# Kernel tuning notes

Hardware: AMD Instinct MI355X
Metric: run time of the kernel (lower is better)

The kernel has to match this reference:

```python
import jax, jax.numpy as jnp
import numpy as np

WS = 8          # window size
NH = 8          # num heads
EPS = 1e-5      # LayerNorm eps (torch default)


def setup_inputs() -> dict:
    key = jax.random.key(0)
    ks = jax.random.split(key, 7)
    B, C, H, W = 16, 256, 128, 128
    x = jax.random.normal(ks[0], (B, C, H, W), dtype=jnp.float32)
    ln_gamma = jnp.ones((C,), dtype=jnp.float32)
    ln_beta = jnp.zeros((C,), dtype=jnp.float32)
    s = 1.0 / np.sqrt(C)
    w_in = jax.random.uniform(ks[1], (3 * C, C), jnp.float32, -s, s)
    b_in = jnp.zeros((3 * C,), dtype=jnp.float32)
    w_out = jax.random.uniform(ks[2], (C, C), jnp.float32, -s, s)
    b_out = jnp.zeros((C,), dtype=jnp.float32)
    return {"x": x, "ln_gamma": ln_gamma, "ln_beta": ln_beta,
            "w_in": w_in, "b_in": b_in, "w_out": w_out, "b_out": b_out}


def _layernorm(x, gamma, beta):
    mu = jnp.mean(x, axis=-1, keepdims=True)
    var = jnp.mean(jnp.square(x - mu), axis=-1, keepdims=True)
    return (x - mu) * jax.lax.rsqrt(var + EPS) * gamma + beta


def reference(x, ln_gamma, ln_beta, w_in, b_in, w_out, b_out):
    B, C, H, W = x.shape
    dh = C // NH
    N = WS * WS
    # (B,C,H,W) -> (B,H,W,C) -> windows (B*nW, N, C)
    xh = jnp.transpose(x, (0, 2, 3, 1))
    win = xh.reshape(B, H // WS, WS, W // WS, WS, C)
    win = jnp.transpose(win, (0, 1, 3, 2, 4, 5)).reshape(-1, N, C)
    # single LayerNorm (the torch code computes the same LN three times)
    xn = _layernorm(win, ln_gamma, ln_beta)
    # fused QKV projection
    qkv = xn @ w_in.T + b_in                      # (Bn, N, 3C)
    q, k, v = jnp.split(qkv, 3, axis=-1)
    def heads(t):
        return jnp.transpose(t.reshape(-1, N, NH, dh), (0, 2, 1, 3))  # (Bn,h,N,dh)
    q, k, v = heads(q), heads(k), heads(v)
    scores = jnp.einsum('bhnd,bhmd->bhnm', q, k) / jnp.sqrt(jnp.float32(dh))
    attn = jax.nn.softmax(scores, axis=-1)
    out = jnp.einsum('bhnm,bhmd->bhnd', attn, v)  # (Bn,h,N,dh)
    out = jnp.transpose(out, (0, 2, 1, 3)).reshape(-1, N, C)
    out = out @ w_out.T + b_out
    # window reverse -> (B,H,W,C) -> (B,C,H,W)
    out = out.reshape(B, H // WS, W // WS, WS, WS, C)
    out = jnp.transpose(out, (0, 1, 3, 2, 4, 5)).reshape(B, H, W, C)
    return jnp.transpose(out, (0, 3, 1, 2))
```

## Files before the change

### kernel.cpp

```cpp
#include <hip/hip_runtime.h>


typedef _Float16 half8  __attribute__((ext_vector_type(8)));
typedef _Float16 half2v __attribute__((ext_vector_type(2)));
typedef float    f32x4  __attribute__((ext_vector_type(4)));

#define XN_STR 264
#define XN_SZ  (64 * XN_STR)
#define S_STR  72
#define S_SZ   (64 * S_STR)
#define SM_TOT (XN_SZ + 4 * S_SZ)

__device__ __forceinline__ int xn_idx(int row, int c) {
    return row * XN_STR + (((c >> 3) ^ (row >> 3)) << 3) + (c & 7);
}
__device__ __forceinline__ int p_idx(int q, int k) {
    return q * 64 + (((k >> 3) ^ (q & 7)) << 3) + (k & 7);
}

__global__ void __launch_bounds__(256)
prep_weights_f16(const float* __restrict__ w_in, const float* __restrict__ w_out,
                 _Float16* __restrict__ wh) {
    int i = blockIdx.x * 256 + threadIdx.x;
    if (i < 196608)      wh[i] = (_Float16)w_in[i];
    else if (i < 262144) wh[i] = (_Float16)w_out[i - 196608];
}

__global__ void __launch_bounds__(256, 2)
win_attn_fused(const float* __restrict__ x, const float* __restrict__ gamma,
               const float* __restrict__ beta, const float* __restrict__ b_in,
               const float* __restrict__ b_out,
               const _Float16* __restrict__ w_in_h,
               const _Float16* __restrict__ w_out_h,
               float* __restrict__ out)
{
    __shared__ __align__(16) _Float16 sm[SM_TOT];
    __shared__ float s_gb[512];

    const int tid  = threadIdx.x;
    const int bidr = blockIdx.x;
    const int wid  = (bidr & 7) * 512 + (bidr >> 3);
    const int b    = wid >> 8;
    const int whi  = (wid >> 4) & 15;
    const int wwi  = wid & 15;
    const int h0 = whi * 8, w0 = wwi * 8;

    s_gb[tid]       = gamma[tid];
    s_gb[256 + tid] = beta[tid];

    const int wv   = tid >> 6;
    const int lane = tid & 63;
    const int quad = lane >> 4;
    const int l16  = lane & 15;

    {
        const int th = lane & 7;
        const int qq = (lane >> 3) & 1;
        const int cg = wv * 4 + (lane >> 4);
        const int t0 = th * 8 + qq * 4;
        const float* xb = x + (((size_t)b * 256) * 128 + h0) * 128 + w0;
#pragma unroll
        for (int it = 0; it < 16; ++it) {
            int c = it * 16 + cg;
            float4 v = *(const float4*)(xb + ((size_t)c * 128 + th) * 128 + qq * 4);
            int base = t0 * XN_STR + (((c >> 3) ^ th) << 3) + (c & 7);
            sm[base]              = (_Float16)v.x;
            sm[base + XN_STR]     = (_Float16)v.y;
            sm[base + 2 * XN_STR] = (_Float16)v.z;
            sm[base + 3 * XN_STR] = (_Float16)v.w;
        }
    }
    __syncthreads();

    {
        const int tok = tid >> 2, cq = tid & 3;
        float sum = 0.f, ss = 0.f;
        half8 hv[8];
#pragma unroll
        for (int k2 = 0; k2 < 8; ++k2) {
            hv[k2] = *(const half8*)&sm[xn_idx(tok, cq * 64 + k2 * 8)];
#pragma unroll
            for (int j = 0; j < 8; ++j) { float f = (float)hv[k2][j]; sum += f; ss += f * f; }
        }
        sum += __shfl_xor(sum, 1); ss += __shfl_xor(ss, 1);
        sum += __shfl_xor(sum, 2); ss += __shfl_xor(ss, 2);
        float mu   = sum * (1.f / 256.f);
        float var  = ss * (1.f / 256.f) - mu * mu;
        float rstd = rsqrtf(var + 1e-5f);
#pragma unroll
        for (int k2 = 0; k2 < 8; ++k2) {
            int c0 = cq * 64 + k2 * 8;
            float4 g0 = *(const float4*)&s_gb[c0];
            float4 g1 = *(const float4*)&s_gb[c0 + 4];
            float4 e0 = *(const float4*)&s_gb[256 + c0];
            float4 e1 = *(const float4*)&s_gb[256 + c0 + 4];
            float gg[8] = {g0.x, g0.y, g0.z, g0.w, g1.x, g1.y, g1.z, g1.w};
            float bb[8] = {e0.x, e0.y, e0.z, e0.w, e1.x, e1.y, e1.z, e1.w};
            half8 o;
#pragma unroll
            for (int j = 0; j < 8; ++j)
                o[j] = (_Float16)(((float)hv[k2][j] - mu) * rstd * gg[j] + bb[j]);
            *(half8*)&sm[xn_idx(tok, c0)] = o;
        }
    }
    __syncthreads();

    const f32x4 zero4 = {0.f, 0.f, 0.f, 0.f};
    _Float16* Swv = &sm[XN_SZ + wv * S_SZ];

    auto qkv_pass = [&](const int p, f32x4 (&acc)[4][4]) {
#pragma unroll
        for (int mt = 0; mt < 4; ++mt)
#pragma unroll
            for (int nt = 0; nt < 4; ++nt) acc[mt][nt] = zero4;
        const _Float16* wb = w_in_h + (size_t)(p * 256 + wv * 64) * 256 + quad * 8;
#pragma unroll
        for (int kb = 0; kb < 256; kb += 32) {
            half8 af[4], bf[4];
#pragma unroll
            for (int mt = 0; mt < 4; ++mt)
                af[mt] = *(const half8*)&sm[xn_idx(mt * 16 + l16, kb + quad * 8)];
#pragma unroll
            for (int nt = 0; nt < 4; ++nt)
                bf[nt] = *(const half8*)(wb + (size_t)(nt * 16 + l16) * 256 + kb);
#pragma unroll
            for (int mt = 0; mt < 4; ++mt)
#pragma unroll
                for (int nt = 0; nt < 4; ++nt)
                    acc[mt][nt] = __builtin_amdgcn_mfma_f32_16x16x32_f16(af[mt], bf[nt], acc[mt][nt], 0, 0, 0);
        }
#pragma unroll
        for (int nt = 0; nt < 4; ++nt) {
            float bi = b_in[p * 256 + wv * 64 + nt * 16 + l16];
#pragma unroll
            for (int mt = 0; mt < 4; ++mt) {
                acc[mt][nt][0] += bi; acc[mt][nt][1] += bi;
                acc[mt][nt][2] += bi; acc[mt][nt][3] += bi;
            }
        }
    };

    half8 qfrag[2][4], kfrag[2][4];

    {
        f32x4 acc[4][4];
        qkv_pass(0, acc);
#pragma unroll
        for (int mt = 0; mt < 4; ++mt)
#pragma unroll
            for (int nt = 0; nt < 4; ++nt)
#pragma unroll
                for (int r = 0; r < 4; ++r)
                    Swv[(mt * 16 + quad * 4 + r) * S_STR + nt * 16 + l16] = (_Float16)acc[mt][nt][r];
        asm volatile("s_waitcnt lgkmcnt(0)" ::: "memory");
        __builtin_amdgcn_sched_barrier(0);
#pragma unroll
        for (int hh = 0; hh < 2; ++hh)
#pragma unroll
            for (int nt = 0; nt < 4; ++nt)
                qfrag[hh][nt] = *(const half8*)&Swv[(nt * 16 + l16) * S_STR + hh * 32 + quad * 8];
    }
    asm volatile("s_waitcnt lgkmcnt(0)" ::: "memory");
    __builtin_amdgcn_sched_barrier(0);

    {
        f32x4 acc[4][4];
        qkv_pass(1, acc);
#pragma unroll
        for (int mt = 0; mt < 4; ++mt)
#pragma unroll
            for (int nt = 0; nt < 4; ++nt)
#pragma unroll
                for (int r = 0; r < 4; ++r)
                    Swv[(mt * 16 + quad * 4 + r) * S_STR + nt * 16 + l16] = (_Float16)acc[mt][nt][r];
        asm volatile("s_waitcnt lgkmcnt(0)" ::: "memory");
        __builtin_amdgcn_sched_barrier(0);
#pragma unroll
        for (int hh = 0; hh < 2; ++hh)
#pragma unroll
            for (int nt = 0; nt < 4; ++nt)
                kfrag[hh][nt] = *(const half8*)&Swv[(nt * 16 + l16) * S_STR + hh * 32 + quad * 8];
    }
    asm volatile("s_waitcnt lgkmcnt(0)" ::: "memory");
    __builtin_amdgcn_sched_barrier(0);

    {
        f32x4 acc[4][4];
        qkv_pass(2, acc);
#pragma unroll
        for (int mt = 0; mt < 4; ++mt)
#pragma unroll
            for (int nt = 0; nt < 4; ++nt)
#pragma unroll
                for (int rp = 0; rp < 2; ++rp) {
                    half2v pk = { (_Float16)acc[mt][nt][2 * rp], (_Float16)acc[mt][nt][2 * rp + 1] };
                    *(half2v*)&Swv[(nt * 16 + l16) * S_STR + mt * 16 + quad * 4 + 2 * rp] = pk;
                }
    }
    __syncthreads();

    f32x4 oacc[2][2][4];
    float rs[2][4];
    _Float16* Pw = &sm[wv * 4096];

#pragma unroll
    for (int hh = 0; hh < 2; ++hh) {
        f32x4 s[4][4];
#pragma unroll
        for (int mt = 0; mt < 4; ++mt)
#pragma unroll
            for (int nt = 0; nt < 4; ++nt)
                s[mt][nt] = __builtin_amdgcn_mfma_f32_16x16x32_f16(kfrag[hh][mt], qfrag[hh][nt], zero4, 0, 0, 0);

        const float SC = 0.17677669529663687f * 1.4426950408889634f;
#pragma unroll
        for (int nt = 0; nt < 4; ++nt) {
            float m = -3.0e38f;
#pragma unroll
            for (int mt = 0; mt < 4; ++mt)
#pragma unroll
                for (int r = 0; r < 4; ++r) m = fmaxf(m, s[mt][nt][r]);
            m = fmaxf(m, __shfl_xor(m, 16));
            m = fmaxf(m, __shfl_xor(m, 32));
            float sum = 0.f;
#pragma unroll
            for (int mt = 0; mt < 4; ++mt)
#pragma unroll
                for (int r = 0; r < 4; ++r) {
                    float e = exp2f((s[mt][nt][r] - m) * SC);
                    s[mt][nt][r] = e; sum += e;
                }
            sum += __shfl_xor(sum, 16);
            sum += __shfl_xor(sum, 32);
            rs[hh][nt] = 1.f / sum;
        }

#pragma unroll
        for (int nt = 0; nt < 4; ++nt) {
            int q = nt * 16 + l16;
#pragma unroll
            for (int mt = 0; mt < 4; ++mt) {
                int k0 = mt * 16 + quad * 4;
                int a0 = p_idx(q, k0);
                half2v lo = { (_Float16)s[mt][nt][0], (_Float16)s[mt][nt][1] };
                half2v hi = { (_Float16)s[mt][nt][2], (_Float16)s[mt][nt][3] };
                *(half2v*)&Pw[a0]     = lo;
                *(half2v*)&Pw[a0 + 2] = hi;
            }
        }
        asm volatile("s_waitcnt lgkmcnt(0)" ::: "memory");
        __builtin_amdgcn_sched_barrier(0);

#pragma unroll
        for (int mtv = 0; mtv < 2; ++mtv)
#pragma unroll
            for (int nt = 0; nt < 4; ++nt) oacc[hh][mtv][nt] = zero4;
#pragma unroll
        for (int kb = 0; kb < 2; ++kb) {
            half8 av[2], bp[4];
#pragma unroll
            for (int mtv = 0; mtv < 2; ++mtv)
                av[mtv] = *(const half8*)&Swv[(hh * 32 + mtv * 16 + l16) * S_STR + kb * 32 + quad * 8];
#pragma unroll
            for (int nt = 0; nt < 4; ++nt)
                bp[nt] = *(const half8*)&Pw[p_idx(nt * 16 + l16, kb * 32 + quad * 8)];
#pragma unroll
            for (int mtv = 0; mtv < 2; ++mtv)
#pragma unroll
                for (int nt = 0; nt < 4; ++nt)
                    oacc[hh][mtv][nt] = __builtin_amdgcn_mfma_f32_16x16x32_f16(av[mtv], bp[nt], oacc[hh][mtv][nt], 0, 0, 0);
        }
    }
    __syncthreads();

#pragma unroll
    for (int hh = 0; hh < 2; ++hh)
#pragma unroll
        for (int mtv = 0; mtv < 2; ++mtv)
#pragma unroll
            for (int nt = 0; nt < 4; ++nt) {
                int tok = nt * 16 + l16;
                int c0  = (2 * wv + hh) * 32 + mtv * 16 + quad * 4;
                float sc = rs[hh][nt];
                int a0 = xn_idx(tok, c0);
                half2v lo = { (_Float16)(oacc[hh][mtv][nt][0] * sc), (_Float16)(oacc[hh][mtv][nt][1] * sc) };
                half2v hi = { (_Float16)(oacc[hh][mtv][nt][2] * sc), (_Float16)(oacc[hh][mtv][nt][3] * sc) };
                *(half2v*)&sm[a0]     = lo;
                *(half2v*)&sm[a0 + 2] = hi;
            }
    __syncthreads();

    f32x4 pacc[4][4];
#pragma unroll
    for (int mt = 0; mt < 4; ++mt)
#pragma unroll
        for (int nt = 0; nt < 4; ++nt) pacc[mt][nt] = zero4;
    const _Float16* wor = w_out_h + (size_t)(64 * wv + l16) * 256 + quad * 8;
#pragma unroll
    for (int kb = 0; kb < 256; kb += 32) {
        half8 aw[4], bo[4];
#pragma unroll
        for (int mt = 0; mt < 4; ++mt) aw[mt] = *(const half8*)(wor + mt * 16 * 256 + kb);
#pragma unroll
        for (int nt = 0; nt < 4; ++nt)
            bo[nt] = *(const half8*)&sm[xn_idx(nt * 16 + l16, kb + quad * 8)];
#pragma unroll
        for (int mt = 0; mt < 4; ++mt)
#pragma unroll
            for (int nt = 0; nt < 4; ++nt)
                pacc[mt][nt] = __builtin_amdgcn_mfma_f32_16x16x32_f16(aw[mt], bo[nt], pacc[mt][nt], 0, 0, 0);
    }

    float* ob = out + (((size_t)b * 256) * 128 + h0) * 128 + w0;
#pragma unroll
    for (int mt = 0; mt < 4; ++mt) {
#pragma unroll
        for (int r = 0; r < 4; ++r) {
            int c = 64 * wv + mt * 16 + quad * 4 + r;
            float bi = b_out[c];
#pragma unroll
            for (int nt = 0; nt < 4; ++nt) {
                int tok = nt * 16 + l16;
                ob[((size_t)c * 128 + (tok >> 3)) * 128 + (tok & 7)] = pacc[mt][nt][r] + bi;
            }
        }
    }
}

extern "C" void kernel_launch(void* const* d_in, const int* in_sizes, int n_in,
                              void* d_out, int out_size, void* d_ws, size_t ws_size,
                              hipStream_t stream) {
    const float* x        = (const float*)d_in[0];
    const float* ln_gamma = (const float*)d_in[1];
    const float* ln_beta  = (const float*)d_in[2];
    const float* w_in     = (const float*)d_in[3];
    const float* b_in     = (const float*)d_in[4];
    const float* w_out    = (const float*)d_in[5];
    const float* b_out    = (const float*)d_in[6];
    float* y = (float*)d_out;

    _Float16* w_in_h  = (_Float16*)d_ws;
    _Float16* w_out_h = w_in_h + 196608;

    prep_weights_f16<<<1024, 256, 0, stream>>>(w_in, w_out, w_in_h);
    win_attn_fused<<<4096, 256, 0, stream>>>(x, ln_gamma, ln_beta, b_in, b_out,
                                             w_in_h, w_out_h, y);
}
```

Before: 694.5 us.

## Replace LDS staging of Q/K/V/P with register ds_bpermute fragment shuffles

Q, K, V and softmax probabilities are rearranged into MFMA operand layouts through cross-lane ds_bpermute shuffles in registers, so the per-wave LDS scratch buffers and their write/read round-trips go away. This shrinks shared memory to the single normalized-activation tile, which lets launch bounds target three blocks per CU instead of two. Softmax normalization now happens before the PV product and attention is processed per head to keep fewer live accumulators. The cost is many extra bpermute instructions and higher register pressure, which could cause spills under the tighter occupancy bound.

```diff
diff --git a/kernel.cpp b/kernel.cpp
--- a/kernel.cpp
+++ b/kernel.cpp
@@ -7,15 +7,25 @@
 
 #define XN_STR 264
 #define XN_SZ  (64 * XN_STR)
-#define S_STR  72
-#define S_SZ   (64 * S_STR)
-#define SM_TOT (XN_SZ + 4 * S_SZ)
 
 __device__ __forceinline__ int xn_idx(int row, int c) {
     return row * XN_STR + (((c >> 3) ^ (row >> 3)) << 3) + (c & 7);
 }
-__device__ __forceinline__ int p_idx(int q, int k) {
-    return q * 64 + (((k >> 3) ^ (q & 7)) << 3) + (k & 7);
+
+__device__ __forceinline__ int pk2(float a, float b) {
+    half2v h = { (_Float16)a, (_Float16)b };
+    return __builtin_bit_cast(int, h);
+}
+
+__device__ __forceinline__ int qsel(bool hi, int idx, int lo_r, int hi_r) {
+    int a = __builtin_amdgcn_ds_bpermute(idx, lo_r);
+    int b = __builtin_amdgcn_ds_bpermute(idx, hi_r);
+    return hi ? b : a;
+}
+
+__device__ __forceinline__ half8 frag4(int w0, int w1, int w2, int w3) {
+    int4 t = { w0, w1, w2, w3 };
+    return __builtin_bit_cast(half8, t);
 }
 
 __global__ void __launch_bounds__(256)
@@ -26,7 +36,7 @@
     else if (i < 262144) wh[i] = (_Float16)w_out[i - 196608];
 }
 
-__global__ void __launch_bounds__(256, 2)
+__global__ void __launch_bounds__(256, 3)
 win_attn_fused(const float* __restrict__ x, const float* __restrict__ gamma,
                const float* __restrict__ beta, const float* __restrict__ b_in,
                const float* __restrict__ b_out,
@@ -34,7 +44,7 @@
                const _Float16* __restrict__ w_out_h,
                float* __restrict__ out)
 {
-    __shared__ __align__(16) _Float16 sm[SM_TOT];
+    __shared__ __align__(16) _Float16 sm[XN_SZ];
     __shared__ float s_gb[512];
 
     const int tid  = threadIdx.x;
@@ -56,18 +66,19 @@
     {
         const int th = lane & 7;
         const int qq = (lane >> 3) & 1;
-        const int cg = wv * 4 + (lane >> 4);
-        const int t0 = th * 8 + qq * 4;
+        const int cp = lane >> 4;
+        const int rowb = th * 8 + qq * 4;
         const float* xb = x + (((size_t)b * 256) * 128 + h0) * 128 + w0;
 #pragma unroll
-        for (int it = 0; it < 16; ++it) {
-            int c = it * 16 + cg;
-            float4 v = *(const float4*)(xb + ((size_t)c * 128 + th) * 128 + qq * 4);
-            int base = t0 * XN_STR + (((c >> 3) ^ th) << 3) + (c & 7);
-            sm[base]              = (_Float16)v.x;
-            sm[base + XN_STR]     = (_Float16)v.y;
-            sm[base + 2 * XN_STR] = (_Float16)v.z;
-            sm[base + 3 * XN_STR] = (_Float16)v.w;
+        for (int it = 0; it < 8; ++it) {
+            int c0 = it * 32 + wv * 8 + cp * 2;
+            float4 v0 = *(const float4*)(xb + ((size_t)c0 * 128 + th) * 128 + qq * 4);
+            float4 v1 = *(const float4*)(xb + ((size_t)(c0 + 1) * 128 + th) * 128 + qq * 4);
+            int base = rowb * XN_STR + (((c0 >> 3) ^ th) << 3) + (c0 & 7);
+            *(half2v*)&sm[base]              = half2v{ (_Float16)v0.x, (_Float16)v1.x };
+            *(half2v*)&sm[base + XN_STR]     = half2v{ (_Float16)v0.y, (_Float16)v1.y };
+            *(half2v*)&sm[base + 2 * XN_STR] = half2v{ (_Float16)v0.z, (_Float16)v1.z };
+            *(half2v*)&sm[base + 3 * XN_STR] = half2v{ (_Float16)v0.w, (_Float16)v1.w };
         }
     }
     __syncthreads();
@@ -90,204 +101,203 @@
 #pragma unroll
         for (int k2 = 0; k2 < 8; ++k2) {
             int c0 = cq * 64 + k2 * 8;
-            float4 g0 = *(const float4*)&s_gb[c0];
-            float4 g1 = *(const float4*)&s_gb[c0 + 4];
-            float4 e0 = *(const float4*)&s_gb[256 + c0];
-            float4 e1 = *(const float4*)&s_gb[256 + c0 + 4];
-            float gg[8] = {g0.x, g0.y, g0.z, g0.w, g1.x, g1.y, g1.z, g1.w};
-            float bb[8] = {e0.x, e0.y, e0.z, e0.w, e1.x, e1.y, e1.z, e1.w};
             half8 o;
 #pragma unroll
             for (int j = 0; j < 8; ++j)
-                o[j] = (_Float16)(((float)hv[k2][j] - mu) * rstd * gg[j] + bb[j]);
+                o[j] = (_Float16)(((float)hv[k2][j] - mu) * rstd * s_gb[c0 + j] + s_gb[256 + c0 + j]);
             *(half8*)&sm[xn_idx(tok, c0)] = o;
         }
     }
     __syncthreads();
 
     const f32x4 zero4 = {0.f, 0.f, 0.f, 0.f};
-    _Float16* Swv = &sm[XN_SZ + wv * S_SZ];
-
-    auto qkv_pass = [&](const int p, f32x4 (&acc)[4][4]) {
+    const int idxA = ((lane & 16) << 3) | ((lane & 15) << 2);
+    const int idxB = idxA + 64;
+    const bool hi2 = (lane & 32) != 0;
+
+    auto gemm_pass = [&](const int p, const bool xn_as_A, f32x4 (&acc)[4][4]) {
+#pragma unroll
+        for (int i = 0; i < 4; ++i)
+#pragma unroll
+            for (int j = 0; j < 4; ++j) acc[i][j] = zero4;
+        const _Float16* wb = w_in_h + ((size_t)(p * 256 + wv * 64 + l16)) * 256 + quad * 8;
+#pragma unroll
+        for (int kb = 0; kb < 8; ++kb) {
+            half8 wf[4], bx[4];
+#pragma unroll
+            for (int i = 0; i < 4; ++i)
+                wf[i] = *(const half8*)(wb + (size_t)i * 16 * 256 + kb * 32);
+#pragma unroll
+            for (int j = 0; j < 4; ++j)
+                bx[j] = *(const half8*)&sm[xn_idx(j * 16 + l16, kb * 32 + quad * 8)];
+            if (xn_as_A) {
+#pragma unroll
+                for (int i = 0; i < 4; ++i)
+#pragma unroll
+                    for (int j = 0; j < 4; ++j)
+                        acc[i][j] = __builtin_amdgcn_mfma_f32_16x16x32_f16(bx[i], wf[j], acc[i][j], 0, 0, 0);
+            } else {
+#pragma unroll
+                for (int i = 0; i < 4; ++i)
+#pragma unroll
+                    for (int j = 0; j < 4; ++j)
+                        acc[i][j] = __builtin_amdgcn_mfma_f32_16x16x32_f16(wf[i], bx[j], acc[i][j], 0, 0, 0);
+            }
+        }
+    };
+
+    half8 qfrag[2][4], kfrag[2][4], vfrag[2][2][2];
+
+    {
+        f32x4 acc[4][4];
+        gemm_pass(0, false, acc);
+#pragma unroll
+        for (int mt = 0; mt < 4; ++mt) {
+            f32x4 bq = *(const f32x4*)&b_in[0 * 256 + wv * 64 + mt * 16 + quad * 4];
+#pragma unroll
+            for (int nt = 0; nt < 4; ++nt) acc[mt][nt] += bq;
+        }
+        int pkq[4][4][2];
 #pragma unroll
         for (int mt = 0; mt < 4; ++mt)
 #pragma unroll
-            for (int nt = 0; nt < 4; ++nt) acc[mt][nt] = zero4;
-        const _Float16* wb = w_in_h + (size_t)(p * 256 + wv * 64) * 256 + quad * 8;
-#pragma unroll
-        for (int kb = 0; kb < 256; kb += 32) {
-            half8 af[4], bf[4];
+            for (int nt = 0; nt < 4; ++nt) {
+                pkq[mt][nt][0] = pk2(acc[mt][nt][0], acc[mt][nt][1]);
+                pkq[mt][nt][1] = pk2(acc[mt][nt][2], acc[mt][nt][3]);
+            }
+#pragma unroll
+        for (int hh = 0; hh < 2; ++hh)
+#pragma unroll
+            for (int nt = 0; nt < 4; ++nt)
+                qfrag[hh][nt] = frag4(
+                    qsel(hi2, idxA, pkq[2*hh][nt][0], pkq[2*hh+1][nt][0]),
+                    qsel(hi2, idxA, pkq[2*hh][nt][1], pkq[2*hh+1][nt][1]),
+                    qsel(hi2, idxB, pkq[2*hh][nt][0], pkq[2*hh+1][nt][0]),
+                    qsel(hi2, idxB, pkq[2*hh][nt][1], pkq[2*hh+1][nt][1]));
+    }
+
+    {
+        f32x4 acc[4][4];
+        gemm_pass(1, false, acc);
+#pragma unroll
+        for (int mt = 0; mt < 4; ++mt) {
+            f32x4 bk = *(const f32x4*)&b_in[1 * 256 + wv * 64 + mt * 16 + quad * 4];
+#pragma unroll
+            for (int nt = 0; nt < 4; ++nt) acc[mt][nt] += bk;
+        }
+        int pkk[4][4][2];
+#pragma unroll
+        for (int mt = 0; mt < 4; ++mt)
+#pragma unroll
+            for (int nt = 0; nt < 4; ++nt) {
+                pkk[mt][nt][0] = pk2(acc[mt][nt][0], acc[mt][nt][1]);
+                pkk[mt][nt][1] = pk2(acc[mt][nt][2], acc[mt][nt][3]);
+            }
+#pragma unroll
+        for (int hh = 0; hh < 2; ++hh)
+#pragma unroll
+            for (int nt = 0; nt < 4; ++nt)
+                kfrag[hh][nt] = frag4(
+                    qsel(hi2, idxA, pkk[2*hh][nt][0], pkk[2*hh+1][nt][0]),
+                    qsel(hi2, idxA, pkk[2*hh][nt][1], pkk[2*hh+1][nt][1]),
+                    qsel(hi2, idxB, pkk[2*hh][nt][0], pkk[2*hh+1][nt][0]),
+                    qsel(hi2, idxB, pkk[2*hh][nt][1], pkk[2*hh+1][nt][1]));
+    }
+
+    {
+        f32x4 acc[4][4];
+        gemm_pass(2, true, acc);
+#pragma unroll
+        for (int nt = 0; nt < 4; ++nt) {
+            float bv = b_in[2 * 256 + wv * 64 + nt * 16 + l16];
+            f32x4 bvv = { bv, bv, bv, bv };
+#pragma unroll
+            for (int mt = 0; mt < 4; ++mt) acc[mt][nt] += bvv;
+        }
+        int pkv[4][4][2];
+#pragma unroll
+        for (int mt = 0; mt < 4; ++mt)
+#pragma unroll
+            for (int nt = 0; nt < 4; ++nt) {
+                pkv[mt][nt][0] = pk2(acc[mt][nt][0], acc[mt][nt][1]);
+                pkv[mt][nt][1] = pk2(acc[mt][nt][2], acc[mt][nt][3]);
+            }
+        __syncthreads();
+#pragma unroll
+        for (int hh = 0; hh < 2; ++hh)
+#pragma unroll
+            for (int mtv = 0; mtv < 2; ++mtv)
+#pragma unroll
+                for (int kb = 0; kb < 2; ++kb)
+                    vfrag[hh][mtv][kb] = frag4(
+                        qsel(hi2, idxA, pkv[2*kb][2*hh+mtv][0], pkv[2*kb+1][2*hh+mtv][0]),
+                        qsel(hi2, idxA, pkv[2*kb][2*hh+mtv][1], pkv[2*kb+1][2*hh+mtv][1]),
+                        qsel(hi2, idxB, pkv[2*kb][2*hh+mtv][0], pkv[2*kb+1][2*hh+mtv][0]),
+                        qsel(hi2, idxB, pkv[2*kb][2*hh+mtv][1], pkv[2*kb+1][2*hh+mtv][1]));
+    }
+
+    const float SC = 0.17677669529663687f * 1.4426950408889634f;
+#pragma unroll
+    for (int hh = 0; hh < 2; ++hh) {
+        f32x4 oacc[2][4];
+#pragma unroll
+        for (int mtv = 0; mtv < 2; ++mtv)
+#pragma unroll
+            for (int nt = 0; nt < 4; ++nt) oacc[mtv][nt] = zero4;
+
+#pragma unroll
+        for (int nt = 0; nt < 4; ++nt) {
+            f32x4 s4[4];
 #pragma unroll
             for (int mt = 0; mt < 4; ++mt)
-                af[mt] = *(const half8*)&sm[xn_idx(mt * 16 + l16, kb + quad * 8)];
-#pragma unroll
-            for (int nt = 0; nt < 4; ++nt)
-                bf[nt] = *(const half8*)(wb + (size_t)(nt * 16 + l16) * 256 + kb);
+                s4[mt] = __builtin_amdgcn_mfma_f32_16x16x32_f16(kfrag[hh][mt], qfrag[hh][nt], zero4, 0, 0, 0);
+            float mx = -3.0e38f;
 #pragma unroll
             for (int mt = 0; mt < 4; ++mt)
 #pragma unroll
-                for (int nt = 0; nt < 4; ++nt)
-                    acc[mt][nt] = __builtin_amdgcn_mfma_f32_16x16x32_f16(af[mt], bf[nt], acc[mt][nt], 0, 0, 0);
-        }
-#pragma unroll
-        for (int nt = 0; nt < 4; ++nt) {
-            float bi = b_in[p * 256 + wv * 64 + nt * 16 + l16];
-#pragma unroll
-            for (int mt = 0; mt < 4; ++mt) {
-                acc[mt][nt][0] += bi; acc[mt][nt][1] += bi;
-                acc[mt][nt][2] += bi; acc[mt][nt][3] += bi;
-            }
-        }
-    };
-
-    half8 qfrag[2][4], kfrag[2][4];
-
-    {
-        f32x4 acc[4][4];
-        qkv_pass(0, acc);
-#pragma unroll
-        for (int mt = 0; mt < 4; ++mt)
-#pragma unroll
-            for (int nt = 0; nt < 4; ++nt)
-#pragma unroll
-                for (int r = 0; r < 4; ++r)
-                    Swv[(mt * 16 + quad * 4 + r) * S_STR + nt * 16 + l16] = (_Float16)acc[mt][nt][r];
-        asm volatile("s_waitcnt lgkmcnt(0)" ::: "memory");
-        __builtin_amdgcn_sched_barrier(0);
-#pragma unroll
-        for (int hh = 0; hh < 2; ++hh)
-#pragma unroll
-            for (int nt = 0; nt < 4; ++nt)
-                qfrag[hh][nt] = *(const half8*)&Swv[(nt * 16 + l16) * S_STR + hh * 32 + quad * 8];
-    }
-    asm volatile("s_waitcnt lgkmcnt(0)" ::: "memory");
-    __builtin_amdgcn_sched_barrier(0);
-
-    {
-        f32x4 acc[4][4];
-        qkv_pass(1, acc);
-#pragma unroll
-        for (int mt = 0; mt < 4; ++mt)
-#pragma unroll
-            for (int nt = 0; nt < 4; ++nt)
-#pragma unroll
-                for (int r = 0; r < 4; ++r)
-                    Swv[(mt * 16 + quad * 4 + r) * S_STR + nt * 16 + l16] = (_Float16)acc[mt][nt][r];
-        asm volatile("s_waitcnt lgkmcnt(0)" ::: "memory");
-        __builtin_amdgcn_sched_barrier(0);
-#pragma unroll
-        for (int hh = 0; hh < 2; ++hh)
-#pragma unroll
-            for (int nt = 0; nt < 4; ++nt)
-                kfrag[hh][nt] = *(const half8*)&Swv[(nt * 16 + l16) * S_STR + hh * 32 + quad * 8];
-    }
-    asm volatile("s_waitcnt lgkmcnt(0)" ::: "memory");
-    __builtin_amdgcn_sched_barrier(0);
-
-    {
-        f32x4 acc[4][4];
-        qkv_pass(2, acc);
-#pragma unroll
-        for (int mt = 0; mt < 4; ++mt)
-#pragma unroll
-            for (int nt = 0; nt < 4; ++nt)
-#pragma unroll
-                for (int rp = 0; rp < 2; ++rp) {
-                    half2v pk = { (_Float16)acc[mt][nt][2 * rp], (_Float16)acc[mt][nt][2 * rp + 1] };
-                    *(half2v*)&Swv[(nt * 16 + l16) * S_STR + mt * 16 + quad * 4 + 2 * rp] = pk;
-                }
-    }
-    __syncthreads();
-
-    f32x4 oacc[2][2][4];
-    float rs[2][4];
-    _Float16* Pw = &sm[wv * 4096];
-
-#pragma unroll
-    for (int hh = 0; hh < 2; ++hh) {
-        f32x4 s[4][4];
-#pragma unroll
-        for (int mt = 0; mt < 4; ++mt)
-#pragma unroll
-            for (int nt = 0; nt < 4; ++nt)
-                s[mt][nt] = __builtin_amdgcn_mfma_f32_16x16x32_f16(kfrag[hh][mt], qfrag[hh][nt], zero4, 0, 0, 0);
-
-        const float SC = 0.17677669529663687f * 1.4426950408889634f;
-#pragma unroll
-        for (int nt = 0; nt < 4; ++nt) {
-            float m = -3.0e38f;
+                for (int r = 0; r < 4; ++r) mx = fmaxf(mx, s4[mt][r]);
+            mx = fmaxf(mx, __shfl_xor(mx, 16));
+            mx = fmaxf(mx, __shfl_xor(mx, 32));
+            float sum = 0.f;
 #pragma unroll
             for (int mt = 0; mt < 4; ++mt)
 #pragma unroll
-                for (int r = 0; r < 4; ++r) m = fmaxf(m, s[mt][nt][r]);
-            m = fmaxf(m, __shfl_xor(m, 16));
-            m = fmaxf(m, __shfl_xor(m, 32));
-            float sum = 0.f;
-#pragma unroll
-            for (int mt = 0; mt < 4; ++mt)
-#pragma unroll
                 for (int r = 0; r < 4; ++r) {
-                    float e = exp2f((s[mt][nt][r] - m) * SC);
-                    s[mt][nt][r] = e; sum += e;
+                    float e = exp2f((s4[mt][r] - mx) * SC);
+                    s4[mt][r] = e; sum += e;
                 }
             sum += __shfl_xor(sum, 16);
             sum += __shfl_xor(sum, 32);
-            rs[hh][nt] = 1.f / sum;
-        }
-
-#pragma unroll
-        for (int nt = 0; nt < 4; ++nt) {
-            int q = nt * 16 + l16;
+            float rs = 1.f / sum;
+            int pks[4][2];
 #pragma unroll
             for (int mt = 0; mt < 4; ++mt) {
-                int k0 = mt * 16 + quad * 4;
-                int a0 = p_idx(q, k0);
-                half2v lo = { (_Float16)s[mt][nt][0], (_Float16)s[mt][nt][1] };
-                half2v hi = { (_Float16)s[mt][nt][2], (_Float16)s[mt][nt][3] };
-                *(half2v*)&Pw[a0]     = lo;
-                *(half2v*)&Pw[a0 + 2] = hi;
-            }
-        }
-        asm volatile("s_waitcnt lgkmcnt(0)" ::: "memory");
-        __builtin_amdgcn_sched_barrier(0);
-
-#pragma unroll
-        for (int mtv = 0; mtv < 2; ++mtv)
-#pragma unroll
-            for (int nt = 0; nt < 4; ++nt) oacc[hh][mtv][nt] = zero4;
-#pragma unroll
-        for (int kb = 0; kb < 2; ++kb) {
-            half8 av[2], bp[4];
-#pragma unroll
-            for (int mtv = 0; mtv < 2; ++mtv)
-                av[mtv] = *(const half8*)&Swv[(hh * 32 + mtv * 16 + l16) * S_STR + kb * 32 + quad * 8];
-#pragma unroll
-            for (int nt = 0; nt < 4; ++nt)
-                bp[nt] = *(const half8*)&Pw[p_idx(nt * 16 + l16, kb * 32 + quad * 8)];
-#pragma unroll
-            for (int mtv = 0; mtv < 2; ++mtv)
-#pragma unroll
-                for (int nt = 0; nt < 4; ++nt)
-                    oacc[hh][mtv][nt] = __builtin_amdgcn_mfma_f32_16x16x32_f16(av[mtv], bp[nt], oacc[hh][mtv][nt], 0, 0, 0);
-        }
-    }
-    __syncthreads();
-
-#pragma unroll
-    for (int hh = 0; hh < 2; ++hh)
+                pks[mt][0] = pk2(s4[mt][0] * rs, s4[mt][1] * rs);
+                pks[mt][1] = pk2(s4[mt][2] * rs, s4[mt][3] * rs);
+            }
+#pragma unroll
+            for (int kb = 0; kb < 2; ++kb) {
+                half8 pf = frag4(
+                    qsel(hi2, idxA, pks[2*kb][0], pks[2*kb+1][0]),
+                    qsel(hi2, idxA, pks[2*kb][1], pks[2*kb+1][1]),
+                    qsel(hi2, idxB, pks[2*kb][0], pks[2*kb+1][0]),
+                    qsel(hi2, idxB, pks[2*kb][1], pks[2*kb+1][1]));
+#pragma unroll
+                for (int mtv = 0; mtv < 2; ++mtv)
+                    oacc[mtv][nt] = __builtin_amdgcn_mfma_f32_16x16x32_f16(vfrag[hh][mtv][kb], pf, oacc[mtv][nt], 0, 0, 0);
+            }
+        }
 #pragma unroll
         for (int mtv = 0; mtv < 2; ++mtv)
 #pragma unroll
             for (int nt = 0; nt < 4; ++nt) {
                 int tok = nt * 16 + l16;
                 int c0  = (2 * wv + hh) * 32 + mtv * 16 + quad * 4;
-                float sc = rs[hh][nt];
-                int a0 = xn_idx(tok, c0);
-                half2v lo = { (_Float16)(oacc[hh][mtv][nt][0] * sc), (_Float16)(oacc[hh][mtv][nt][1] * sc) };
-                half2v hi = { (_Float16)(oacc[hh][mtv][nt][2] * sc), (_Float16)(oacc[hh][mtv][nt][3] * sc) };
-                *(half2v*)&sm[a0]     = lo;
-                *(half2v*)&sm[a0 + 2] = hi;
-            }
+                int a0  = xn_idx(tok, c0);
+                *(half2v*)&sm[a0]     = half2v{ (_Float16)oacc[mtv][nt][0], (_Float16)oacc[mtv][nt][1] };
+                *(half2v*)&sm[a0 + 2] = half2v{ (_Float16)oacc[mtv][nt][2], (_Float16)oacc[mtv][nt][3] };
+            }
+    }
     __syncthreads();
 
     f32x4 pacc[4][4];
```

New measurement: 2.129 ms. 3.07x slower.
